# Kernel tuning notes

Hardware: AMD Instinct MI355X
Metric: run time of the kernel (lower is better)

The kernel has to match this reference:

```python
import jax, jax.numpy as jnp
import numpy as np

H, HKV, DH, T_MAX = 32, 8, 128, 4096
ROPE_BASE = 500000.0


def apply_rope(x, pos, base):
    # x: [B, h, T, D]; MLX rope, traditional=False (split-half rotation)
    B, h, T, D = x.shape
    half = D // 2
    inv_freq = 1.0 / (base ** (jnp.arange(half, dtype=jnp.float32) * 2.0 / D))
    t = (pos + jnp.arange(T)).astype(jnp.float32)  # absolute positions
    ang = t[:, None] * inv_freq[None, :]           # [T, half]
    cos = jnp.cos(ang)[None, None]                 # [1,1,T,half]
    sin = jnp.sin(ang)[None, None]
    x1, x2 = x[..., :half], x[..., half:]
    return jnp.concatenate([x1 * cos - x2 * sin, x2 * cos + x1 * sin], axis=-1)


def setup_inputs() -> dict:
    key = jax.random.key(0)
    ks = jax.random.split(key, 5)
    hidden = 4096
    return {
        "hidden_states": jax.random.normal(ks[0], (1, 2048, hidden), jnp.float32),
        "Wq": jax.random.normal(ks[1], (hidden, H * DH), jnp.float32) * 0.02,
        "Wk": jax.random.normal(ks[2], (hidden, HKV * DH), jnp.float32) * 0.02,
        "Wv": jax.random.normal(ks[3], (hidden, HKV * DH), jnp.float32) * 0.02,
        "Wo": jax.random.normal(ks[4], (H * DH, hidden), jnp.float32) * 0.02,
        "pos_int": 0,
    }


def reference(hidden_states, Wq, Wk, Wv, Wo, pos_int):
    B, T, _ = hidden_states.shape
    q = (hidden_states @ Wq).reshape(B, T, H, DH).transpose(0, 2, 1, 3)    # [B,H,T,D]
    k = (hidden_states @ Wk).reshape(B, T, HKV, DH).transpose(0, 2, 1, 3)  # [B,Hkv,T,D]
    v = (hidden_states @ Wv).reshape(B, T, HKV, DH).transpose(0, 2, 1, 3)

    q = apply_rope(q, pos_int, ROPE_BASE)
    k = apply_rope(k, pos_int, ROPE_BASE)

    # KV cache: write at [pos:pos+T], then slice [:pos+T] (pos is static Python int)
    k_cache = jnp.zeros((B, HKV, T_MAX, DH), jnp.float32)
    v_cache = jnp.zeros((B, HKV, T_MAX, DH), jnp.float32)
    k_cache = jax.lax.dynamic_update_slice(k_cache, k, (0, 0, pos_int, 0))
    v_cache = jax.lax.dynamic_update_slice(v_cache, v, (0, 0, pos_int, 0))
    end_pos = pos_int + T
    k_ = k_cache[:, :, :end_pos, :]  # [B,Hkv,S,D]
    v_ = v_cache[:, :, :end_pos, :]
    S = end_pos

    # GQA without materializing repeat_interleave: group query heads per kv head
    group = H // HKV
    qg = q.reshape(B, HKV, group, T, DH)
    scale = 1.0 / jnp.sqrt(jnp.float32(DH))
    scores = jnp.einsum("bhgtd,bhsd->bhgts", qg, k_) * scale  # [B,Hkv,g,T,S]
    # torch SDPA is_causal=True: top-left aligned mask (allow s <= t)
    causal = jnp.arange(S)[None, :] <= jnp.arange(T)[:, None]  # [T,S]
    scores = jnp.where(causal[None, None, None], scores, -jnp.inf)
    probs = jax.nn.softmax(scores, axis=-1)
    attn = jnp.einsum("bhgts,bhsd->bhgtd", probs, v_)          # [B,Hkv,g,T,D]
    attn = attn.reshape(B, H, T, DH).transpose(0, 2, 1, 3).reshape(B, T, H * DH)
    return attn @ Wo
```

## Files before the change

### kernel.cpp

```cpp
#include <hip/hip_runtime.h>
#include <hip/hip_bf16.h>
#include <math.h>

typedef unsigned short u16;
typedef __attribute__((ext_vector_type(4))) float f32x4;
typedef __attribute__((ext_vector_type(8))) short bf16x8;

#define GLD16(gptr, lptr) __builtin_amdgcn_global_load_lds( \
    (const __attribute__((address_space(1))) void*)(gptr),  \
    (__attribute__((address_space(3))) void*)(lptr), 16, 0, 0)

__device__ __forceinline__ float bf2f(u16 u) {
  union { unsigned int i; float f; } c; c.i = ((unsigned int)u) << 16; return c.f;
}
__device__ __forceinline__ u16 f2bf(float f) {
  union { float f; unsigned int i; } c; c.f = f;
  unsigned int r = c.i + 0x7fffu + ((c.i >> 16) & 1u);
  return (u16)(r >> 16);
}

__global__ __launch_bounds__(256) void f32_to_bf16(const float* __restrict__ in,
                                                   u16* __restrict__ out, int n4) {
  int i = blockIdx.x * 256 + threadIdx.x;
  if (i >= n4) return;
  float4 v = reinterpret_cast<const float4*>(in)[i];
  ushort4 o;
  o.x = f2bf(v.x); o.y = f2bf(v.y); o.z = f2bf(v.z); o.w = f2bf(v.w);
  reinterpret_cast<ushort4*>(out)[i] = o;
}

__global__ __launch_bounds__(256) void transpose_qkv_w(const float* __restrict__ Wq,
                                                       const float* __restrict__ Wk,
                                                       const float* __restrict__ Wv,
                                                       u16* __restrict__ WT) {
  __shared__ float tile[32][33];
  const int bx = blockIdx.x, k0 = blockIdx.y * 32;
  const float* W; int n0, N; size_t outbase;
  if (bx < 128)      { W = Wq; n0 = bx * 32;          N = 4096; outbase = 0; }
  else if (bx < 160) { W = Wk; n0 = (bx - 128) * 32;  N = 1024; outbase = (size_t)4096 * 4096; }
  else               { W = Wv; n0 = (bx - 160) * 32;  N = 1024; outbase = (size_t)5120 * 4096; }
  const int tx = threadIdx.x & 31, ty = threadIdx.x >> 5;
#pragma unroll
  for (int r = 0; r < 32; r += 8)
    tile[ty + r][tx] = W[(size_t)(k0 + ty + r) * N + (n0 + tx)];
  __syncthreads();
#pragma unroll
  for (int r = 0; r < 32; r += 8)
    WT[outbase + (size_t)(n0 + ty + r) * 4096 + (k0 + tx)] = f2bf(tile[tx][ty + r]);
}

__global__ __launch_bounds__(256) void transpose_convert(const float* __restrict__ W,
                                                         u16* __restrict__ Wt,
                                                         int K, int N) {
  __shared__ float tile[32][33];
  const int n0 = blockIdx.x * 32, k0 = blockIdx.y * 32;
  const int tx = threadIdx.x & 31, ty = threadIdx.x >> 5;
#pragma unroll
  for (int r = 0; r < 32; r += 8)
    tile[ty + r][tx] = W[(size_t)(k0 + ty + r) * N + (n0 + tx)];
  __syncthreads();
#pragma unroll
  for (int r = 0; r < 32; r += 8)
    Wt[(size_t)(n0 + ty + r) * K + (k0 + tx)] = f2bf(tile[tx][ty + r]);
}

__global__ __launch_bounds__(256) void transpose_v(const u16* __restrict__ Vsrc,
                                                   u16* __restrict__ Vt) {
  __shared__ u16 tile[32][33];
  const int t0 = blockIdx.x * 32, d0 = blockIdx.y * 32, hkv = blockIdx.z;
  const int tx = threadIdx.x & 31, ty = threadIdx.x >> 5;
#pragma unroll
  for (int r = 0; r < 32; r += 8)
    tile[ty + r][tx] = Vsrc[(size_t)(t0 + ty + r) * 6144 + hkv * 128 + d0 + tx];
  __syncthreads();
#pragma unroll
  for (int r = 0; r < 32; r += 8)
    Vt[((size_t)hkv * 128 + d0 + ty + r) * 2048 + t0 + tx] = tile[tx][ty + r];
}

__global__ __launch_bounds__(256) void rope_table(float2* __restrict__ tab,
                                                  const int* __restrict__ pos_ptr) {
  int idx = blockIdx.x * 256 + threadIdx.x;
  int d = idx & 63, t = idx >> 6;
  int pos = *pos_ptr;
  float inv = exp2f(-(float)d * (0.015625f * 18.931568569324174f));
  float ang = (float)(pos + t) * inv;
  tab[idx] = make_float2(cosf(ang), sinf(ang));
}

__global__ __launch_bounds__(256) void rope_apply_qk(u16* __restrict__ QKV,
                                                     const float2* __restrict__ tab) {
  int idx = blockIdx.x * 256 + threadIdx.x;
  if (idx >= 2048 * 40 * 64) return;
  int d = idx & 63;
  int hh = (idx >> 6) % 40;
  int t = idx / (64 * 40);
  float2 cs = tab[t * 64 + d];
  const int col = (hh < 32) ? hh * 128 : 4096 + (hh - 32) * 128;
  size_t base = (size_t)t * 6144 + col + d;
  float x1 = bf2f(QKV[base]);
  float x2 = bf2f(QKV[base + 64]);
  QKV[base]      = f2bf(x1 * cs.x - x2 * cs.y);
  QKV[base + 64] = f2bf(x2 * cs.x + x1 * cs.y);
}

template <int BN, int OUT_BF16>
__global__ __launch_bounds__(512, 4) void gemm_2cu(const u16* __restrict__ A,
                                                   const u16* __restrict__ Bt,
                                                   void* __restrict__ C,
                                                   int M, int N, int K) {
  constexpr int NF = BN / 64;
  constexpr int WCOL = BN / 4;
  constexpr int LB = BN / 64;
  __shared__ alignas(16) u16 As[2][128 * 64];
  __shared__ alignas(16) u16 Bs[2][BN * 64];
  const int tid = threadIdx.x;
  const int lane = tid & 63, wid = tid >> 6;
  const int l15 = lane & 15, lg = lane >> 4;
  const int wm = wid >> 2, wn = wid & 3;
  const int wvb = tid & ~63;

  const int gy = gridDim.y;
  const int id0 = blockIdx.y * gridDim.x + blockIdx.x;
  const int xcd = id0 & 7;
  const int l = id0 >> 3;
  const int m0 = (l % gy) * 128;
  const int n0 = (xcd * (gridDim.x >> 3) + l / gy) * BN;

  f32x4 acc[4][NF];
#pragma unroll
  for (int i = 0; i < 4; ++i)
#pragma unroll
    for (int j = 0; j < NF; ++j) {
      f32x4 zz = {0.f, 0.f, 0.f, 0.f};
      acc[i][j] = zz;
    }

#define STAGE(s_, b_)                                                           \
  do {                                                                          \
    _Pragma("unroll")                                                           \
    for (int p = 0; p < 2; ++p) {                                               \
      const int slot = p * 512 + tid;                                           \
      const int row = slot >> 3, ch = slot & 7;                                 \
      const int col = (ch ^ (row & 7)) * 8;                                     \
      GLD16(A + (size_t)(m0 + row) * K + (s_) * 64 + col,                       \
            &As[b_][(p * 512 + wvb) * 8]);                                      \
    }                                                                           \
    _Pragma("unroll")                                                           \
    for (int p = 0; p < LB; ++p) {                                              \
      const int slot = p * 512 + tid;                                           \
      const int row = slot >> 3, ch = slot & 7;                                 \
      const int col = (ch ^ (row & 7)) * 8;                                     \
      GLD16(Bt + (size_t)(n0 + row) * K + (s_) * 64 + col,                      \
            &Bs[b_][(p * 512 + wvb) * 8]);                                      \
    }                                                                           \
  } while (0)

  STAGE(0, 0);
  __syncthreads();
  int cur = 0;

  const int nt = K >> 6;
  for (int t = 0; t < nt; ++t) {
    if (t + 1 < nt) STAGE(t + 1, cur ^ 1);
#pragma unroll
    for (int g = 0; g < 2; ++g) {
      bf16x8 af[4], bfr[NF];
#pragma unroll
      for (int i = 0; i < 4; ++i) {
        const int row = wm * 64 + i * 16 + l15;
        const int ch = (g * 4 + lg) ^ (row & 7);
        af[i] = *reinterpret_cast<const bf16x8*>(&As[cur][row * 64 + ch * 8]);
      }
#pragma unroll
      for (int j = 0; j < NF; ++j) {
        const int row = wn * WCOL + j * 16 + l15;
        const int ch = (g * 4 + lg) ^ (row & 7);
        bfr[j] = *reinterpret_cast<const bf16x8*>(&Bs[cur][row * 64 + ch * 8]);
      }
      __builtin_amdgcn_s_setprio(1);
#pragma unroll
      for (int i = 0; i < 4; ++i)
#pragma unroll
        for (int j = 0; j < NF; ++j)
          acc[i][j] = __builtin_amdgcn_mfma_f32_16x16x32_bf16(af[i], bfr[j], acc[i][j], 0, 0, 0);
      __builtin_amdgcn_s_setprio(0);
    }
    __syncthreads();
    cur ^= 1;
  }
#undef STAGE

#pragma unroll
  for (int i = 0; i < 4; ++i)
#pragma unroll
    for (int j = 0; j < NF; ++j)
#pragma unroll
      for (int r = 0; r < 4; ++r) {
        const int row = m0 + wm * 64 + i * 16 + lg * 4 + r;
        const int col = n0 + wn * WCOL + j * 16 + l15;
        const float v = acc[i][j][r];
        if (OUT_BF16) ((u16*)C)[(size_t)row * N + col] = f2bf(v);
        else          ((float*)C)[(size_t)row * N + col] = v;
      }
}

__global__ __launch_bounds__(512, 4) void attn_kernel(const u16* __restrict__ Q,
                                                      const u16* __restrict__ K,
                                                      const u16* __restrict__ Vt,
                                                      u16* __restrict__ O,
                                                      const int* __restrict__ pos_ptr) {
  const int pos = *pos_ptr;
  const int id = (int)blockIdx.x;
  const int hq = id & 255;
  const int h = hq >> 3;
  const int qb = (id < 256) ? (15 - (hq & 7)) : (hq & 7);
  const int hkv = h >> 2;
  const int tid = threadIdx.x;
  const int w = tid >> 6, lane = tid & 63;
  const int l15 = lane & 15, lg = lane >> 4;

  __shared__ alignas(16) u16 Ks[2][64 * 128];
  __shared__ alignas(16) u16 Vs[2][128 * 64];
  __shared__ alignas(16) u16 Pl[8][16][40];

  const u16* Kh = K + hkv * 128;
  const u16* Vh = Vt + (size_t)hkv * 128 * 2048;

  const float C = 0.12752961957823275f;
  const float THR = 62.0f;
  const int wvb = tid & ~63;

#define STAGE_TILE(st_, b_)                                                        \
  do {                                                                             \
    const int s0_ = (st_) * 64;                                                    \
    _Pragma("unroll")                                                              \
    for (int p = 0; p < 2; ++p) {                                                  \
      const int idx = p * 512 + tid;                                               \
      const int kr = idx >> 4, kc = (idx & 15) ^ (kr & 7);                         \
      GLD16(Kh + (size_t)(s0_ + kr) * 6144 + kc * 8, &Ks[b_][(p * 512 + wvb) * 8]);\
      const int vr = idx >> 3, vc = (idx & 7) ^ (vr & 7);                          \
      GLD16(Vh + (size_t)vr * 2048 + s0_ + vc * 8, &Vs[b_][(p * 512 + wvb) * 8]);  \
    }                                                                              \
  } while (0)

  const int qt0 = qb * 128;
  const int nst = 2 * qb + 2;
  const int frag_base = qt0 + w * 16;

  bf16x8 qa[4];
#pragma unroll
  for (int kk = 0; kk < 4; ++kk)
    qa[kk] = *reinterpret_cast<const bf16x8*>(
        Q + (size_t)(frag_base + l15) * 6144 + h * 128 + kk * 32 + lg * 8);

  f32x4 acc[8];
#pragma unroll
  for (int i = 0; i < 8; ++i) { f32x4 z = {0.f, 0.f, 0.f, 0.f}; acc[i] = z; }
  float mrun[4], lpart[4];
#pragma unroll
  for (int r = 0; r < 4; ++r) {
    mrun[r] = (pos > 0) ? 0.0f : -INFINITY;
    lpart[r] = 0.0f;
  }

  STAGE_TILE(0, 0);
  __syncthreads();
  int cur = 0;

  for (int st = 0; st < nst; ++st) {
    if (st + 1 < nst) STAGE_TILE(st + 1, cur ^ 1);
    const int s0 = st * 64;

    float pv[4][4];
    __builtin_amdgcn_s_setprio(1);
#pragma unroll
    for (int sub = 0; sub < 4; ++sub) {
      f32x4 s4 = {0.f, 0.f, 0.f, 0.f};
      const int row = sub * 16 + l15;
#pragma unroll
      for (int kk = 0; kk < 4; ++kk) {
        const int chunk = (kk * 4 + lg) ^ (row & 7);
        bf16x8 kf = *reinterpret_cast<const bf16x8*>(&Ks[cur][row * 128 + chunk * 8]);
        s4 = __builtin_amdgcn_mfma_f32_16x16x32_bf16(qa[kk], kf, s4, 0, 0, 0);
      }
#pragma unroll
      for (int r = 0; r < 4; ++r) pv[sub][r] = s4[r];
    }
    __builtin_amdgcn_s_setprio(0);

    if (s0 + 64 > frag_base) {
#pragma unroll
      for (int r = 0; r < 4; ++r) {
        const int qrow = frag_base + lg * 4 + r;
#pragma unroll
        for (int sub = 0; sub < 4; ++sub) {
          const int scol = s0 + sub * 16 + l15;
          pv[sub][r] = (scol <= qrow) ? pv[sub][r] : -INFINITY;
        }
      }
    }

    float dml = -INFINITY;
#pragma unroll
    for (int r = 0; r < 4; ++r)
      dml = fmaxf(dml, fmaxf(fmaxf(pv[0][r], pv[1][r]),
                             fmaxf(pv[2][r], pv[3][r])) - mrun[r]);
    if (!__all(dml <= THR)) {
      float sfr[4];
#pragma unroll
      for (int r = 0; r < 4; ++r) {
        float mx = fmaxf(fmaxf(pv[0][r], pv[1][r]), fmaxf(pv[2][r], pv[3][r]));
#pragma unroll
        for (int off = 1; off < 16; off <<= 1) mx = fmaxf(mx, __shfl_xor(mx, off));
        const float mnew = fmaxf(mrun[r], mx);
        sfr[r] = exp2f((mrun[r] - mnew) * C);
        mrun[r] = mnew;
        lpart[r] *= sfr[r];
      }
#pragma unroll
      for (int dc = 0; dc < 8; ++dc)
#pragma unroll
        for (int r = 0; r < 4; ++r) acc[dc][r] *= sfr[r];
    }

#pragma unroll
    for (int half = 0; half < 2; ++half) {
#pragma unroll
      for (int r = 0; r < 4; ++r) {
        const float nmC = -mrun[r] * C;
        float ps = 0.0f;
#pragma unroll
        for (int s2 = 0; s2 < 2; ++s2) {
          const int sub = half * 2 + s2;
          const float p = exp2f(fmaf(pv[sub][r], C, nmC));
          pv[sub][r] = p;
          ps += p;
        }
        lpart[r] += ps;
      }
#pragma unroll
      for (int s2 = 0; s2 < 2; ++s2)
#pragma unroll
        for (int r = 0; r < 4; ++r)
          Pl[w][lg * 4 + r][s2 * 16 + l15] = f2bf(pv[half * 2 + s2][r]);

      bf16x8 pf = *reinterpret_cast<const bf16x8*>(&Pl[w][l15][lg * 8]);
      __builtin_amdgcn_s_setprio(1);
#pragma unroll
      for (int dc = 0; dc < 8; ++dc) {
        const int row = dc * 16 + l15;
        const int chunk = (half * 4 + lg) ^ (row & 7);
        bf16x8 vf = *reinterpret_cast<const bf16x8*>(&Vs[cur][row * 64 + chunk * 8]);
        acc[dc] = __builtin_amdgcn_mfma_f32_16x16x32_bf16(pf, vf, acc[dc], 0, 0, 0);
      }
      __builtin_amdgcn_s_setprio(0);
    }

    __syncthreads();
    cur ^= 1;
  }

#pragma unroll
  for (int r = 0; r < 4; ++r) {
    float l = lpart[r];
#pragma unroll
    for (int off = 1; off < 16; off <<= 1) l += __shfl_xor(l, off);
    if (pos > 0) l += (float)pos * exp2f(-mrun[r] * C);
    const float linv = 1.0f / l;
    const int qrow = frag_base + lg * 4 + r;
#pragma unroll
    for (int dc = 0; dc < 8; ++dc)
      O[(size_t)qrow * 4096 + h * 128 + dc * 16 + l15] = f2bf(acc[dc][r] * linv);
  }
#undef STAGE_TILE
}

extern "C" void kernel_launch(void* const* d_in, const int* in_sizes, int n_in,
                              void* d_out, int out_size, void* d_ws, size_t ws_size,
                              hipStream_t stream) {
  const float* hs = (const float*)d_in[0];
  const float* Wq = (const float*)d_in[1];
  const float* Wk = (const float*)d_in[2];
  const float* Wv = (const float*)d_in[3];
  const float* Wo = (const float*)d_in[4];
  const int* pos  = (const int*)d_in[5];

  char* ws = (char*)d_ws;
  u16* hs_bf = (u16*)(ws + 0);
  u16* WT    = (u16*)(ws + 16777216ULL);
  u16* QKVb  = (u16*)(ws + 67108864ULL);
  u16* attnO = hs_bf;
  u16* WoT   = WT;
  u16* Vtg   = (u16*)(ws + 50331648ULL);
  float2* tabF = (float2*)(ws + 54525952ULL);

  f32_to_bf16<<<8192, 256, 0, stream>>>(hs, hs_bf, 2097152);
  transpose_qkv_w<<<dim3(192, 128), 256, 0, stream>>>(Wq, Wk, Wv, WT);

  gemm_2cu<192, 1><<<dim3(32, 16), 512, 0, stream>>>(hs_bf, WT, QKVb, 2048, 6144, 4096);

  transpose_convert<<<dim3(128, 128), 256, 0, stream>>>(Wo, WoT, 4096, 4096);

  rope_table<<<512, 256, 0, stream>>>(tabF, pos);
  rope_apply_qk<<<20480, 256, 0, stream>>>(QKVb, tabF);

  transpose_v<<<dim3(64, 4, 8), 256, 0, stream>>>(QKVb + 5120, Vtg);

  attn_kernel<<<dim3(512), 512, 0, stream>>>(QKVb, QKVb + 4096, Vtg, attnO, pos);

  gemm_2cu<128, 0><<<dim3(32, 16), 512, 0, stream>>>(attnO, WoT, d_out, 2048, 4096, 4096);
}
```

Before: 331.9 us.

## Fuse Q RoPE into attention and split-K the output projection GEMM

Q RoPE is now applied to the query fragments inside the attention kernel, so the standalone rope pass only handles K heads and moves less memory. The final Wo GEMM becomes a split-K kernel with 128x256 tiles and K-chunks of 32, writing two bf16 partial products, which a new reduce kernel sums into the fp32 output. The goal is a larger grid and better CU occupancy for the output GEMM. The costs are extra partial-buffer traffic, an added launch, and bf16 rounding of the partial sums before accumulation, which lowers output precision.

```diff
diff --git a/kernel.cpp b/kernel.cpp
--- a/kernel.cpp
+++ b/kernel.cpp
@@ -88,16 +88,15 @@
   tab[idx] = make_float2(cosf(ang), sinf(ang));
 }
 
-__global__ __launch_bounds__(256) void rope_apply_qk(u16* __restrict__ QKV,
-                                                     const float2* __restrict__ tab) {
+__global__ __launch_bounds__(256) void rope_apply_k(u16* __restrict__ QKV,
+                                                    const float2* __restrict__ tab) {
   int idx = blockIdx.x * 256 + threadIdx.x;
-  if (idx >= 2048 * 40 * 64) return;
+  if (idx >= 2048 * 8 * 64) return;
   int d = idx & 63;
-  int hh = (idx >> 6) % 40;
-  int t = idx / (64 * 40);
+  int hh = (idx >> 6) & 7;
+  int t = idx >> 9;
   float2 cs = tab[t * 64 + d];
-  const int col = (hh < 32) ? hh * 128 : 4096 + (hh - 32) * 128;
-  size_t base = (size_t)t * 6144 + col + d;
+  size_t base = (size_t)t * 6144 + 4096 + hh * 128 + d;
   float x1 = bf2f(QKV[base]);
   float x2 = bf2f(QKV[base + 64]);
   QKV[base]      = f2bf(x1 * cs.x - x2 * cs.y);
@@ -205,11 +204,124 @@
       }
 }
 
+__global__ __launch_bounds__(512, 4) void gemm_wo(const u16* __restrict__ A,
+                                                  const u16* __restrict__ Bt,
+                                                  u16* __restrict__ P,
+                                                  int M, int N, int K,
+                                                  int ntiles, size_t zstride) {
+  __shared__ alignas(16) u16 As[2][128 * 32];
+  __shared__ alignas(16) u16 Bs[2][256 * 32];
+  const int tid = threadIdx.x;
+  const int lane = tid & 63, wid = tid >> 6;
+  const int l15 = lane & 15, lg = lane >> 4;
+  const int wm = wid >> 2, wn = wid & 3;
+  const int wvb = tid & ~63;
+  const int z = blockIdx.z;
+  const int ko = z * ntiles * 32;
+
+  const int id0 = blockIdx.y * gridDim.x + blockIdx.x;
+  const int xcd = id0 & 7;
+  const int l = id0 >> 3;
+  const int m0 = (l % gridDim.y) * 128;
+  const int n0 = (xcd * (gridDim.x >> 3) + l / gridDim.y) * 256;
+
+  f32x4 acc[4][4];
+#pragma unroll
+  for (int i = 0; i < 4; ++i)
+#pragma unroll
+    for (int j = 0; j < 4; ++j) {
+      f32x4 zz = {0.f, 0.f, 0.f, 0.f};
+      acc[i][j] = zz;
+    }
+
+#define SW32(row_) (((row_) >> 1) & 3)
+#define STAGE(s_, b_)                                                           \
+  do {                                                                          \
+    {                                                                           \
+      const int row = tid >> 2, ch = tid & 3;                                   \
+      const int col = (ch ^ SW32(row)) * 8;                                     \
+      GLD16(A + (size_t)(m0 + row) * K + ko + (s_) * 32 + col,                  \
+            &As[b_][wvb * 8]);                                                  \
+    }                                                                           \
+    _Pragma("unroll")                                                           \
+    for (int p = 0; p < 2; ++p) {                                               \
+      const int slot = p * 512 + tid;                                           \
+      const int row = slot >> 2, ch = slot & 3;                                 \
+      const int col = (ch ^ SW32(row)) * 8;                                     \
+      GLD16(Bt + (size_t)(n0 + row) * K + ko + (s_) * 32 + col,                 \
+            &Bs[b_][(p * 512 + wvb) * 8]);                                      \
+    }                                                                           \
+  } while (0)
+
+  STAGE(0, 0);
+  __syncthreads();
+  int cur = 0;
+
+  for (int t = 0; t < ntiles; ++t) {
+    if (t + 1 < ntiles) STAGE(t + 1, cur ^ 1);
+    bf16x8 af[4], bfr[4];
+#pragma unroll
+    for (int i = 0; i < 4; ++i) {
+      const int row = wm * 64 + i * 16 + l15;
+      const int ch = lg ^ SW32(row);
+      af[i] = *reinterpret_cast<const bf16x8*>(&As[cur][row * 32 + ch * 8]);
+    }
+#pragma unroll
+    for (int j = 0; j < 4; ++j) {
+      const int row = wn * 64 + j * 16 + l15;
+      const int ch = lg ^ SW32(row);
+      bfr[j] = *reinterpret_cast<const bf16x8*>(&Bs[cur][row * 32 + ch * 8]);
+    }
+    __builtin_amdgcn_s_setprio(1);
+#pragma unroll
+    for (int i = 0; i < 4; ++i)
+#pragma unroll
+      for (int j = 0; j < 4; ++j)
+        acc[i][j] = __builtin_amdgcn_mfma_f32_16x16x32_bf16(af[i], bfr[j], acc[i][j], 0, 0, 0);
+    __builtin_amdgcn_s_setprio(0);
+    __syncthreads();
+    cur ^= 1;
+  }
+#undef STAGE
+#undef SW32
+
+  u16* Pb = P + (size_t)z * zstride;
+#pragma unroll
+  for (int i = 0; i < 4; ++i)
+#pragma unroll
+    for (int j = 0; j < 4; ++j)
+#pragma unroll
+      for (int r = 0; r < 4; ++r) {
+        const int row = m0 + wm * 64 + i * 16 + lg * 4 + r;
+        const int col = n0 + wn * 64 + j * 16 + l15;
+        Pb[(size_t)row * N + col] = f2bf(acc[i][j][r]);
+      }
+}
+
+__global__ __launch_bounds__(256) void wo_reduce(const u16* __restrict__ P,
+                                                 float* __restrict__ out) {
+  const size_t i = ((size_t)blockIdx.x * 256 + threadIdx.x) * 8;
+  bf16x8 a = *reinterpret_cast<const bf16x8*>(P + i);
+  bf16x8 b = *reinterpret_cast<const bf16x8*>(P + 8388608 + i);
+  float4 o0, o1;
+  o0.x = bf2f((u16)a[0]) + bf2f((u16)b[0]);
+  o0.y = bf2f((u16)a[1]) + bf2f((u16)b[1]);
+  o0.z = bf2f((u16)a[2]) + bf2f((u16)b[2]);
+  o0.w = bf2f((u16)a[3]) + bf2f((u16)b[3]);
+  o1.x = bf2f((u16)a[4]) + bf2f((u16)b[4]);
+  o1.y = bf2f((u16)a[5]) + bf2f((u16)b[5]);
+  o1.z = bf2f((u16)a[6]) + bf2f((u16)b[6]);
+  o1.w = bf2f((u16)a[7]) + bf2f((u16)b[7]);
+  *reinterpret_cast<float4*>(out + i) = o0;
+  *reinterpret_cast<float4*>(out + i + 4) = o1;
+}
+
 __global__ __launch_bounds__(512, 4) void attn_kernel(const u16* __restrict__ Q,
                                                       const u16* __restrict__ K,
                                                       const u16* __restrict__ Vt,
                                                       u16* __restrict__ O,
-                                                      const int* __restrict__ pos_ptr) {
+                                                      const int* __restrict__ pos_ptr,
+                                                      const float2* __restrict__ tab) {
   const int pos = *pos_ptr;
   const int id = (int)blockIdx.x;
   const int hq = id & 255;
@@ -254,6 +366,21 @@
     qa[kk] = *reinterpret_cast<const bf16x8*>(
         Q + (size_t)(frag_base + l15) * 6144 + h * 128 + kk * 32 + lg * 8);
 
+  {
+    const float2* tb = tab + (size_t)(frag_base + l15) * 64;
+#pragma unroll
+    for (int kk = 0; kk < 2; ++kk)
+#pragma unroll
+      for (int e = 0; e < 8; ++e) {
+        const int d = kk * 32 + lg * 8 + e;
+        const float2 cs = tb[d];
+        const float x1 = bf2f((u16)qa[kk][e]);
+        const float x2 = bf2f((u16)qa[kk + 2][e]);
+        qa[kk][e]     = (short)f2bf(x1 * cs.x - x2 * cs.y);
+        qa[kk + 2][e] = (short)f2bf(x2 * cs.x + x1 * cs.y);
+      }
+  }
+
   f32x4 acc[8];
 #pragma unroll
   for (int i = 0; i < 8; ++i) { f32x4 z = {0.f, 0.f, 0.f, 0.f}; acc[i] = z; }
@@ -394,6 +521,7 @@
   u16* WoT   = WT;
   u16* Vtg   = (u16*)(ws + 50331648ULL);
   float2* tabF = (float2*)(ws + 54525952ULL);
+  u16* Ppart = (u16*)(ws + 50331648ULL);
 
   f32_to_bf16<<<8192, 256, 0, stream>>>(hs, hs_bf, 2097152);
   transpose_qkv_w<<<dim3(192, 128), 256, 0, stream>>>(Wq, Wk, Wv, WT);
@@ -403,11 +531,13 @@
   transpose_convert<<<dim3(128, 128), 256, 0, stream>>>(Wo, WoT, 4096, 4096);
 
   rope_table<<<512, 256, 0, stream>>>(tabF, pos);
-  rope_apply_qk<<<20480, 256, 0, stream>>>(QKVb, tabF);
+  rope_apply_k<<<4096, 256, 0, stream>>>(QKVb, tabF);
 
   transpose_v<<<dim3(64, 4, 8), 256, 0, stream>>>(QKVb + 5120, Vtg);
 
-  attn_kernel<<<dim3(512), 512, 0, stream>>>(QKVb, QKVb + 4096, Vtg, attnO, pos);
-
-  gemm_2cu<128, 0><<<dim3(32, 16), 512, 0, stream>>>(attnO, WoT, d_out, 2048, 4096, 4096);
-}
+  attn_kernel<<<dim3(512), 512, 0, stream>>>(QKVb, QKVb + 4096, Vtg, attnO, pos, tabF);
+
+  gemm_wo<<<dim3(16, 16, 2), 512, 0, stream>>>(attnO, WoT, Ppart, 2048, 4096, 4096,
+                                               64, 8388608);
+  wo_reduce<<<4096, 256, 0, stream>>>(Ppart, (float*)d_out);
+}
```

New measurement: 340.2 us. 2.5% more time.
